# Kernel optimization log

Hardware: AMD Instinct MI355X
Metric: run time of the kernel (lower is better)

## Reference

```python
import jax, jax.numpy as jnp
import numpy as np
import math

IN_DIM = 256
OUT_DIM = 256
H = 4
DK = OUT_DIM // H  # 64
N = 40000
E = 300000
T = 2  # node types
R = 3  # relations: 0:(A->B), 1:(B->A), 2:(A->B)


def setup_inputs() -> dict:
    key = jax.random.key(0)
    ks = jax.random.split(key, 24)
    def xavier(k, shape):
        fan_in, fan_out = shape[-2], shape[-1]
        lim = math.sqrt(6.0 / (fan_in + fan_out))
        return jax.random.uniform(k, shape, jnp.float32, -lim, lim)
    inp = {
        "hA": jax.random.normal(ks[0], (N, IN_DIM), jnp.float32),
        "hB": jax.random.normal(ks[1], (N, IN_DIM), jnp.float32),
        "src0": jax.random.randint(ks[2], (E,), 0, N, jnp.int32),
        "dst0": jax.random.randint(ks[3], (E,), 0, N, jnp.int32),
        "src1": jax.random.randint(ks[4], (E,), 0, N, jnp.int32),
        "dst1": jax.random.randint(ks[5], (E,), 0, N, jnp.int32),
        "src2": jax.random.randint(ks[6], (E,), 0, N, jnp.int32),
        "dst2": jax.random.randint(ks[7], (E,), 0, N, jnp.int32),
        # per-node-type linear weights, stacked [T, in, out]
        "Wk": xavier(ks[8], (T, IN_DIM, OUT_DIM)),
        "bk": jnp.zeros((T, OUT_DIM), jnp.float32),
        "Wq": xavier(ks[9], (T, IN_DIM, OUT_DIM)),
        "bq": jnp.zeros((T, OUT_DIM), jnp.float32),
        "Wv": xavier(ks[10], (T, IN_DIM, OUT_DIM)),
        "bv": jnp.zeros((T, OUT_DIM), jnp.float32),
        "Wa": xavier(ks[11], (T, OUT_DIM, OUT_DIM)),
        "ba": jnp.zeros((T, OUT_DIM), jnp.float32),
        "rel_att": xavier(ks[12], (R, H, DK, DK)),
        "rel_msg": xavier(ks[13], (R, H, DK, DK)),
        "rel_pri": jnp.ones((R, H), jnp.float32),
        "skip": jnp.ones((T,), jnp.float32),
    }
    return inp


def _hgt_forward(hA, hB, Wk, bk, Wq, bq, Wv, bv, Wa, ba,
                 rel_att, rel_msg, rel_pri, skip, edges):
    h = [hA, hB]
    sqrt_dk = math.sqrt(DK)

    def proj(W, b, x, t):
        return (x @ W[t] + b[t]).reshape(-1, H, DK)

    def rel_agg(r, s, d, src, dst):
        # relation-specific transforms
        k = jnp.einsum('nhi,hij->nhj', proj(Wk, bk, h[s], s), rel_att[r])
        v = jnp.einsum('nhi,hij->nhj', proj(Wv, bv, h[s], s), rel_msg[r])
        q = proj(Wq, bq, h[d], d)
        nd = h[d].shape[0]
        # per-edge dot-product attention score [E, H]
        score = jnp.einsum('ehd,ehd->eh', q[dst], k[src]) * rel_pri[r] / sqrt_dk
        # edge softmax normalized by destination node
        m = jax.ops.segment_max(score, dst, num_segments=nd)
        e = jnp.exp(score - m[dst])
        denom = jax.ops.segment_sum(e, dst, num_segments=nd)
        attn = e / denom[dst]
        # weighted scatter-sum aggregation -> [nd, H, DK]
        return jax.ops.segment_sum(v[src] * attn[:, :, None], dst, num_segments=nd)

    (src0, dst0), (src1, dst1), (src2, dst2) = edges
    agg0 = rel_agg(0, 0, 1, src0, dst0)  # A -> B
    agg1 = rel_agg(1, 1, 0, src1, dst1)  # B -> A
    agg2 = rel_agg(2, 0, 1, src2, dst2)  # A -> B

    # cross_reducer='mean' over etypes per destination type
    t_A = agg1.reshape(-1, OUT_DIM)
    t_B = ((agg0 + agg2) * 0.5).reshape(-1, OUT_DIM)

    def ts_aggr(t, n_id, h_dst):
        alpha = jax.nn.sigmoid(skip[n_id])
        trans = t @ Wa[n_id] + ba[n_id]  # dropout p=0.0 -> identity
        return trans * alpha + h_dst * (1.0 - alpha)

    out_A = ts_aggr(t_A, 0, hA)
    out_B = ts_aggr(t_B, 1, hB)
    return jnp.stack([out_A, out_B])  # [2, N, OUT_DIM]


def reference(hA, hB, src0, dst0, src1, dst1, src2, dst2,
              Wk, bk, Wq, bq, Wv, bv, Wa, ba,
              rel_att, rel_msg, rel_pri, skip):
    edges = ((src0, dst0), (src1, dst1), (src2, dst2))
    return _hgt_forward(hA, hB, Wk, bk, Wq, bq, Wv, bv, Wa, ba,
                        rel_att, rel_msg, rel_pri, skip, edges)
```

## Files before the change

kernel.cpp:

```cpp
#include <hip/hip_runtime.h>

#define NN 40000
#define EE 300000
#define DIM 256
#define NHD 4
#define CAP 64

typedef __attribute__((ext_vector_type(8))) short bfrag;
typedef __attribute__((ext_vector_type(4))) float fx4;

static __device__ __forceinline__ float bf2f(unsigned short u) {
  union { unsigned int i; float f; } v; v.i = ((unsigned int)u) << 16; return v.f;
}
static __device__ __forceinline__ unsigned short f2bf(float f) {
  union { float f; unsigned int i; } v; v.f = f;
  unsigned int x = v.i;
  return (unsigned short)((x + 0x7fffu + ((x >> 16) & 1u)) >> 16);
}
static __device__ __forceinline__ void unpack4(uint2 u, float f[4]) {
  f[0] = bf2f((unsigned short)(u.x & 0xffffu));
  f[1] = bf2f((unsigned short)(u.x >> 16));
  f[2] = bf2f((unsigned short)(u.y & 0xffffu));
  f[3] = bf2f((unsigned short)(u.y >> 16));
}
static __device__ __forceinline__ void unpackKV(uint4 u, float k[4], float v[4]) {
  k[0] = bf2f((unsigned short)(u.x & 0xffffu)); k[1] = bf2f((unsigned short)(u.x >> 16));
  k[2] = bf2f((unsigned short)(u.y & 0xffffu)); k[3] = bf2f((unsigned short)(u.y >> 16));
  v[0] = bf2f((unsigned short)(u.z & 0xffffu)); v[1] = bf2f((unsigned short)(u.z >> 16));
  v[2] = bf2f((unsigned short)(u.w & 0xffffu)); v[3] = bf2f((unsigned short)(u.w >> 16));
}
static __device__ __forceinline__ void gload_lds16(const unsigned short* g, unsigned short* l) {
  __builtin_amdgcn_global_load_lds((const __attribute__((address_space(1))) void*)g,
                                   (__attribute__((address_space(3))) void*)l, 16, 0, 0);
}

#define LDSBUF 16384
static __device__ __forceinline__ void gemm_core(const unsigned short* __restrict__ X,
                                                 const unsigned short* __restrict__ WT,
                                                 int R0, int C0, int rowMax,
                                                 fx4 acc[4][4],
                                                 unsigned short* lds) {
  const int tid = threadIdx.x;
  const int wave = tid >> 6, lane = tid & 63;
  const int li = lane & 15, lk = lane >> 4;
  const int wr = wave >> 1, wc = wave & 1;
  const int lr = lane >> 3;
  const int swz = ((lane & 7) ^ lr) * 8;

#define STAGE(KT, BUF)                                                          \
  {                                                                             \
    unsigned short* lA = lds + (BUF) * LDSBUF;                                  \
    unsigned short* lB = lA + 8192;                                             \
    const int k0 = (KT) * 64;                                                   \
    _Pragma("unroll")                                                           \
    for (int i = 0; i < 4; ++i) {                                               \
      int g = wave * 4 + i;                                                     \
      int ra = min(R0 + g * 8 + lr, rowMax);                                    \
      gload_lds16(X + (size_t)ra * DIM + k0 + swz, lA + g * 512);               \
      int cb = C0 + g * 8 + lr;                                                 \
      gload_lds16(WT + (size_t)cb * DIM + k0 + swz, lB + g * 512);              \
    }                                                                           \
  }

  STAGE(0, 0);
#pragma unroll
  for (int kt = 0; kt < 4; ++kt) {
    __syncthreads();
    if (kt < 3) STAGE(kt + 1, (kt + 1) & 1);
    unsigned short* lA = lds + (kt & 1) * LDSBUF;
    unsigned short* lB = lA + 8192;
#pragma unroll
    for (int ks = 0; ks < 2; ++ks) {
      bfrag a[4], b[4];
      const int chb = (lk + ks * 4) ^ (li & 7);
#pragma unroll
      for (int mt = 0; mt < 4; ++mt)
        a[mt] = *(const bfrag*)(lA + (wr * 64 + mt * 16 + li) * 64 + chb * 8);
#pragma unroll
      for (int nt = 0; nt < 4; ++nt)
        b[nt] = *(const bfrag*)(lB + (wc * 64 + nt * 16 + li) * 64 + chb * 8);
#pragma unroll
      for (int mt = 0; mt < 4; ++mt)
#pragma unroll
        for (int nt = 0; nt < 4; ++nt)
          acc[mt][nt] = __builtin_amdgcn_mfma_f32_16x16x32_bf16(a[mt], b[nt], acc[mt][nt], 0, 0, 0);
    }
  }
#undef STAGE
}

__global__ __launch_bounds__(256) void cvt_kernel(const float* __restrict__ hA,
                                                  const float* __restrict__ hB,
                                                  unsigned short* __restrict__ XA,
                                                  unsigned short* __restrict__ XB) {
  long id = (long)blockIdx.x * 256 + threadIdx.x;
  const long half = (long)NN * DIM / 8;
  const float4* src; unsigned short* dst; long o;
  if (id < half) { src = (const float4*)hA; dst = XA; o = id; }
  else           { src = (const float4*)hB; dst = XB; o = id - half; }
  float4 a = src[o * 2], b = src[o * 2 + 1];
  uint4 pk;
  pk.x = (unsigned)f2bf(a.x) | ((unsigned)f2bf(a.y) << 16);
  pk.y = (unsigned)f2bf(a.z) | ((unsigned)f2bf(a.w) << 16);
  pk.z = (unsigned)f2bf(b.x) | ((unsigned)f2bf(b.y) << 16);
  pk.w = (unsigned)f2bf(b.z) | ((unsigned)f2bf(b.w) << 16);
  ((uint4*)dst)[o] = pk;
}

__global__ __launch_bounds__(256) void prep_weights(
    const float* __restrict__ Wk, const float* __restrict__ bk,
    const float* __restrict__ Wq, const float* __restrict__ bq,
    const float* __restrict__ Wv, const float* __restrict__ bv,
    const float* __restrict__ Wa,
    const float* __restrict__ rel_att, const float* __restrict__ rel_msg,
    const float* __restrict__ rel_pri,
    unsigned short* __restrict__ WT_A, unsigned short* __restrict__ WT_B,
    unsigned short* __restrict__ WaT, float* __restrict__ biasA, float* __restrict__ biasB) {
  int id = blockIdx.x * 256 + threadIdx.x;
  if (id < 262144) {
    int c = id >> 8, i = id & 255;
    int br = c >> 9, w = c & 511, h = w >> 7, ww = w & 127;
    int iskv = (ww >> 2) & 1;
    int j = (ww >> 3) * 4 + (ww & 3);
    int r = br ? 2 : 0;
    const float* W  = iskv ? Wv : Wk;
    const float* RM = iskv ? rel_msg : rel_att;
    const float* wrow = W + i * 256 + h * 64;
    const float* rm = RM + (size_t)((r * NHD + h) * 64) * 64 + j;
    float s = 0.f;
#pragma unroll 8
    for (int l = 0; l < 64; l++) s += wrow[l] * rm[l * 64];
    if (!iskv) s *= rel_pri[r * NHD + h] * 0.125f;
    WT_A[c * 256 + i] = f2bf(s);
    return;
  }
  id -= 262144;
  if (id < 65536) {
    int c = id >> 8, i = id & 255;
    WT_A[(1024 + c) * 256 + i] = f2bf(Wq[i * 256 + c]);
    return;
  }
  id -= 65536;
  if (id < 131072) {
    int c = id >> 8, i = id & 255;
    int h = c >> 7, ww = c & 127;
    int iskv = (ww >> 2) & 1;
    int j = (ww >> 3) * 4 + (ww & 3);
    const float* W  = iskv ? Wv : Wk;
    const float* RM = iskv ? rel_msg : rel_att;
    const float* wrow = W + 65536 + i * 256 + h * 64;
    const float* rm = RM + (size_t)((1 * NHD + h) * 64) * 64 + j;
    float s = 0.f;
#pragma unroll 8
    for (int l = 0; l < 64; l++) s += wrow[l] * rm[l * 64];
    if (!iskv) s *= rel_pri[1 * NHD + h] * 0.125f;
    WT_B[c * 256 + i] = f2bf(s);
    return;
  }
  id -= 131072;
  if (id < 65536) {
    int c = id >> 8, i = id & 255;
    WT_B[(512 + c) * 256 + i] = f2bf(Wq[65536 + i * 256 + c]);
    return;
  }
  id -= 65536;
  if (id < 131072) {
    int t = id >> 16, rem = id & 65535, c = rem >> 8, i = rem & 255;
    WaT[t * 65536 + c * 256 + i] = f2bf(Wa[t * 65536 + i * 256 + c]);
    return;
  }
  id -= 131072;
  if (id < 2048) {
    if (id < 1280) {
      int c = id; float s;
      if (c < 1024) {
        int br = c >> 9, w = c & 511, h = w >> 7, ww = w & 127;
        int iskv = (ww >> 2) & 1;
        int j = (ww >> 3) * 4 + (ww & 3);
        int r = br ? 2 : 0;
        const float* B  = iskv ? bv : bk;
        const float* RM = iskv ? rel_msg : rel_att;
        s = 0.f;
        for (int l = 0; l < 64; l++)
          s += B[h * 64 + l] * RM[(size_t)((r * NHD + h) * 64 + l) * 64 + j];
        if (!iskv) s *= rel_pri[r * NHD + h] * 0.125f;
      } else s = bq[c - 1024];
      biasA[c] = s;
    } else {
      int c = id - 1280; float s;
      if (c < 512) {
        int h = c >> 7, ww = c & 127;
        int iskv = (ww >> 2) & 1;
        int j = (ww >> 3) * 4 + (ww & 3);
        const float* B  = iskv ? bv : bk;
        const float* RM = iskv ? rel_msg : rel_att;
        s = 0.f;
        for (int l = 0; l < 64; l++)
          s += B[256 + h * 64 + l] * RM[(size_t)((1 * NHD + h) * 64 + l) * 64 + j];
        if (!iskv) s *= rel_pri[1 * NHD + h] * 0.125f;
      } else s = bq[256 + (c - 512)];
      biasB[c] = s;
    }
  }
}

__global__ __launch_bounds__(256) void bucket_build(const int* __restrict__ src0, const int* __restrict__ dst0,
                                                    const int* __restrict__ src1, const int* __restrict__ dst1,
                                                    const int* __restrict__ src2, const int* __restrict__ dst2,
                                                    int* __restrict__ cnt, int* __restrict__ bkt) {
  int e = blockIdx.x * 256 + threadIdx.x;
  if (e >= EE) return;
  int r = blockIdx.y;
  const int* src = r == 0 ? src0 : (r == 1 ? src1 : src2);
  const int* dst = r == 0 ? dst0 : (r == 1 ? dst1 : dst2);
  int d = dst[e];
  int pos = atomicAdd(&cnt[r * NN + d], 1);
  if (pos < CAP) bkt[(size_t)r * NN * CAP + d * CAP + pos] = src[e];
}

__global__ __launch_bounds__(256) void gemm_kvq(const unsigned short* __restrict__ X,
                                                const unsigned short* __restrict__ WT,
                                                const float* __restrict__ bias,
                                                unsigned short* __restrict__ Out, int ldOut) {
  __shared__ unsigned short lds[2 * LDSBUF];
  fx4 acc[4][4] = {};
  const int R0 = blockIdx.x * 128, C0 = blockIdx.y * 128;
  gemm_core(X, WT, R0, C0, NN - 1, acc, lds);
  const int wave = threadIdx.x >> 6, lane = threadIdx.x & 63;
  const int li = lane & 15, lk = lane >> 4;
  const int wr = wave >> 1, wc = wave & 1;
#pragma unroll
  for (int mt = 0; mt < 4; mt++)
#pragma unroll
    for (int nt = 0; nt < 4; nt++) {
      int col = C0 + wc * 64 + nt * 16 + li;
      float bcol = bias[col];
      int rbase = R0 + wr * 64 + mt * 16 + lk * 4;
#pragma unroll
      for (int i = 0; i < 4; i++) {
        int row = rbase + i;
        if (row < NN) Out[(long)row * ldOut + col] = f2bf(acc[mt][nt][i] + bcol);
      }
    }
}

__global__ __launch_bounds__(256) void agg_all(const unsigned short* __restrict__ OutA,
                                               const unsigned short* __restrict__ OutB,
                                               const int* __restrict__ cnt,
                                               const int* __restrict__ bkt,
                                               unsigned short* __restrict__ tA,
                                               unsigned short* __restrict__ tB) {
  int wid = (blockIdx.x * 256 + threadIdx.x) >> 6;
  int lane = threadIdx.x & 63;
  int h = lane >> 4, li = lane & 15;
  int qoff = h * 64 + li * 4;
  int kvoff = h * 128 + li * 8;
  if (wid < NN) {
    int n = wid;
    float q[4]; unpack4(*(const uint2*)(OutB + (size_t)n * 768 + 512 + qoff), q);
    int c0 = min(cnt[n], CAP);
    int c2 = min(cnt[2 * NN + n], CAP);
    int s0 = (lane < c0) ? bkt[(size_t)0 * NN * CAP + n * CAP + lane] : 0;
    int s2 = (lane < c2) ? bkt[(size_t)2 * NN * CAP + n * CAP + lane] : 0;
    float l0 = 0.f, l2 = 0.f;
    float b00 = 0.f, b01 = 0.f, b02 = 0.f, b03 = 0.f;
    float b20 = 0.f, b21 = 0.f, b22 = 0.f, b23 = 0.f;
    int cm = max(c0, c2);
    for (int e = 0; e < cm; ++e) {
      if (e < c0) {
        int src = __builtin_amdgcn_readlane(s0, e);
        uint4 u = *(const uint4*)(OutA + (size_t)src * 1280 + kvoff);
        float kk[4], vv[4]; unpackKV(u, kk, vv);
        float pp = q[0] * kk[0] + q[1] * kk[1] + q[2] * kk[2] + q[3] * kk[3];
        pp += __shfl_xor(pp, 1); pp += __shfl_xor(pp, 2);
        pp += __shfl_xor(pp, 4); pp += __shfl_xor(pp, 8);
        float p = __expf(pp);
        l0 += p; b00 += p * vv[0]; b01 += p * vv[1]; b02 += p * vv[2]; b03 += p * vv[3];
      }
      if (e < c2) {
        int src = __builtin_amdgcn_readlane(s2, e);
        uint4 u = *(const uint4*)(OutA + (size_t)src * 1280 + 512 + kvoff);
        float kk[4], vv[4]; unpackKV(u, kk, vv);
        float pp = q[0] * kk[0] + q[1] * kk[1] + q[2] * kk[2] + q[3] * kk[3];
        pp += __shfl_xor(pp, 1); pp += __shfl_xor(pp, 2);
        pp += __shfl_xor(pp, 4); pp += __shfl_xor(pp, 8);
        float p = __expf(pp);
        l2 += p; b20 += p * vv[0]; b21 += p * vv[1]; b22 += p * vv[2]; b23 += p * vv[3];
      }
    }
    float i0 = (l0 > 0.f) ? 0.5f / l0 : 0.f;
    float i2 = (l2 > 0.f) ? 0.5f / l2 : 0.f;
    float r0 = b00 * i0 + b20 * i2, r1 = b01 * i0 + b21 * i2;
    float r2 = b02 * i0 + b22 * i2, r3 = b03 * i0 + b23 * i2;
    uint2 pk;
    pk.x = (unsigned)f2bf(r0) | ((unsigned)f2bf(r1) << 16);
    pk.y = (unsigned)f2bf(r2) | ((unsigned)f2bf(r3) << 16);
    *(uint2*)(tB + (size_t)n * DIM + qoff) = pk;
  } else if (wid < 2 * NN) {
    int n = wid - NN;
    float q[4]; unpack4(*(const uint2*)(OutA + (size_t)n * 1280 + 1024 + qoff), q);
    int c = min(cnt[NN + n], CAP);
    int s1 = (lane < c) ? bkt[(size_t)1 * NN * CAP + n * CAP + lane] : 0;
    float l = 0.f, a0 = 0.f, a1 = 0.f, a2 = 0.f, a3 = 0.f;
    int e = 0;
    for (; e + 1 < c; e += 2) {
      int sa = __builtin_amdgcn_readlane(s1, e);
      int sb = __builtin_amdgcn_readlane(s1, e + 1);
      uint4 ua = *(const uint4*)(OutB + (size_t)sa * 768 + kvoff);
      uint4 ub = *(const uint4*)(OutB + (size_t)sb * 768 + kvoff);
      float ka[4], va[4], kb[4], vb[4];
      unpackKV(ua, ka, va); unpackKV(ub, kb, vb);
      float pa = q[0] * ka[0] + q[1] * ka[1] + q[2] * ka[2] + q[3] * ka[3];
      float pb = q[0] * kb[0] + q[1] * kb[1] + q[2] * kb[2] + q[3] * kb[3];
      pa += __shfl_xor(pa, 1); pa += __shfl_xor(pa, 2);
      pa += __shfl_xor(pa, 4); pa += __shfl_xor(pa, 8);
      pb += __shfl_xor(pb, 1); pb += __shfl_xor(pb, 2);
      pb += __shfl_xor(pb, 4); pb += __shfl_xor(pb, 8);
      pa = __expf(pa); pb = __expf(pb);
      l += pa; l += pb;
      a0 += pa * va[0]; a1 += pa * va[1]; a2 += pa * va[2]; a3 += pa * va[3];
      a0 += pb * vb[0]; a1 += pb * vb[1]; a2 += pb * vb[2]; a3 += pb * vb[3];
    }
    if (e < c) {
      int sa = __builtin_amdgcn_readlane(s1, e);
      uint4 ua = *(const uint4*)(OutB + (size_t)sa * 768 + kvoff);
      float ka[4], va[4]; unpackKV(ua, ka, va);
      float pa = q[0] * ka[0] + q[1] * ka[1] + q[2] * ka[2] + q[3] * ka[3];
      pa += __shfl_xor(pa, 1); pa += __shfl_xor(pa, 2);
      pa += __shfl_xor(pa, 4); pa += __shfl_xor(pa, 8);
      pa = __expf(pa);
      l += pa;
      a0 += pa * va[0]; a1 += pa * va[1]; a2 += pa * va[2]; a3 += pa * va[3];
    }
    float inv = (l > 0.f) ? 1.f / l : 0.f;
    uint2 pk;
    pk.x = (unsigned)f2bf(a0 * inv) | ((unsigned)f2bf(a1 * inv) << 16);
    pk.y = (unsigned)f2bf(a2 * inv) | ((unsigned)f2bf(a3 * inv) << 16);
    *(uint2*)(tA + (size_t)n * DIM + qoff) = pk;
  }
}

__global__ __launch_bounds__(256) void gemm_final2(const unsigned short* __restrict__ tA,
                                                   const unsigned short* __restrict__ tB,
                                                   const unsigned short* __restrict__ XA,
                                                   const unsigned short* __restrict__ XB,
                                                   const unsigned short* __restrict__ WaT,
                                                   const float* __restrict__ ba,
                                                   const float* __restrict__ skip,
                                                   float* __restrict__ outp) {
  __shared__ unsigned short lds[2 * LDSBUF];
  const int t = blockIdx.z;
  const unsigned short* Tt = t ? tB : tA;
  const unsigned short* hin = t ? XB : XA;
  float* op = outp + (size_t)t * NN * DIM;
  fx4 acc[4][4] = {};
  const int R0 = blockIdx.x * 128, C0 = blockIdx.y * 128;
  gemm_core(Tt, WaT + t * 65536, R0, C0, NN - 1, acc, lds);
  const int wave = threadIdx.x >> 6, lane = threadIdx.x & 63;
  const int li = lane & 15, lk = lane >> 4;
  const int wr = wave >> 1, wc = wave & 1;
  float alpha = 1.f / (1.f + __expf(-skip[t]));
  float beta = 1.f - alpha;
#pragma unroll
  for (int mt = 0; mt < 4; mt++)
#pragma unroll
    for (int nt = 0; nt < 4; nt++) {
      int col = C0 + wc * 64 + nt * 16 + li;
      float bcol = ba[t * 256 + col];
      int rbase = R0 + wr * 64 + mt * 16 + lk * 4;
#pragma unroll
      for (int i = 0; i < 4; i++) {
        int row = rbase + i;
        if (row < NN) {
          float hv = bf2f(hin[(size_t)row * DIM + col]);
          op[(long)row * DIM + col] = (acc[mt][nt][i] + bcol) * alpha + hv * beta;
        }
      }
    }
}

extern "C" void kernel_launch(void* const* d_in, const int* in_sizes, int n_in,
                              void* d_out, int out_size, void* d_ws, size_t ws_size,
                              hipStream_t stream) {
  const float* hA = (const float*)d_in[0];
  const float* hB = (const float*)d_in[1];
  const int* src0 = (const int*)d_in[2];
  const int* dst0 = (const int*)d_in[3];
  const int* src1 = (const int*)d_in[4];
  const int* dst1 = (const int*)d_in[5];
  const int* src2 = (const int*)d_in[6];
  const int* dst2 = (const int*)d_in[7];
  const float* Wk = (const float*)d_in[8];
  const float* bk = (const float*)d_in[9];
  const float* Wq = (const float*)d_in[10];
  const float* bq = (const float*)d_in[11];
  const float* Wv = (const float*)d_in[12];
  const float* bv = (const float*)d_in[13];
  const float* Wa = (const float*)d_in[14];
  const float* ba = (const float*)d_in[15];
  const float* rel_att = (const float*)d_in[16];
  const float* rel_msg = (const float*)d_in[17];
  const float* rel_pri = (const float*)d_in[18];
  const float* skip = (const float*)d_in[19];

  char* w = (char*)d_ws;
  unsigned short* XA   = (unsigned short*)(w);
  unsigned short* XB   = (unsigned short*)(w + 20480000);
  unsigned short* OutA = (unsigned short*)(w + 40960000);
  unsigned short* OutB = (unsigned short*)(w + 143360000);
  unsigned short* WT_A = (unsigned short*)(w + 204800000);
  unsigned short* WT_B = (unsigned short*)(w + 205455360);
  unsigned short* WaT  = (unsigned short*)(w + 205848576);
  float* biasA = (float*)(w + 206110720);
  float* biasB = (float*)(w + 206115840);
  int* cnt  = (int*)(w + 206118912);
  int* bkt  = (int*)(w + 206598912);
  unsigned short* tA = (unsigned short*)(w + 237318912);
  unsigned short* tB = (unsigned short*)(w + 257798912);

  hipMemsetAsync(cnt, 0, 3 * NN * sizeof(int), stream);
  cvt_kernel<<<10000, 256, 0, stream>>>(hA, hB, XA, XB);
  prep_weights<<<2568, 256, 0, stream>>>(Wk, bk, Wq, bq, Wv, bv, Wa,
                                         rel_att, rel_msg, rel_pri,
                                         WT_A, WT_B, WaT, biasA, biasB);
  bucket_build<<<dim3((EE + 255) / 256, 3), 256, 0, stream>>>(src0, dst0, src1, dst1, src2, dst2, cnt, bkt);
  gemm_kvq<<<dim3(313, 10), 256, 0, stream>>>(XA, WT_A, biasA, OutA, 1280);
  gemm_kvq<<<dim3(313, 6), 256, 0, stream>>>(XB, WT_B, biasB, OutB, 768);
  agg_all<<<20000, 256, 0, stream>>>(OutA, OutB, cnt, bkt, tA, tB);
  gemm_final2<<<dim3(313, 2, 2), 256, 0, stream>>>(tA, tB, XA, XB, WaT, ba, skip, (float*)d_out);
}
```

Measured before the change: 441.2 us.

## Shrink GEMM row tiles to 64 and software-pipeline gathers in aggregation

The GEMM kernels now use 64-row tiles with a single LDS buffer and no double-buffered prefetch. Because 40000 divides evenly by 64, the row bounds checks are dropped, and the grid doubles to fill more CUs with lower LDS use per block. The aggregation kernel now issues K/V gathers for the next edges before processing the current ones, two or four deep, to hide gather latency. The trade-off is losing the overlap of global-to-LDS loads with MFMA inside each GEMM block.

```diff
diff --git a/kernel.cpp b/kernel.cpp
--- a/kernel.cpp
+++ b/kernel.cpp
@@ -34,59 +34,46 @@
                                    (__attribute__((address_space(3))) void*)l, 16, 0, 0);
 }
 
-#define LDSBUF 16384
-static __device__ __forceinline__ void gemm_core(const unsigned short* __restrict__ X,
-                                                 const unsigned short* __restrict__ WT,
-                                                 int R0, int C0, int rowMax,
-                                                 fx4 acc[4][4],
-                                                 unsigned short* lds) {
+static __device__ __forceinline__ void gemm_core64(const unsigned short* __restrict__ X,
+                                                   const unsigned short* __restrict__ WT,
+                                                   int R0, int C0,
+                                                   fx4 acc[2][4],
+                                                   unsigned short* ldsA,
+                                                   unsigned short* ldsB) {
   const int tid = threadIdx.x;
   const int wave = tid >> 6, lane = tid & 63;
   const int li = lane & 15, lk = lane >> 4;
   const int wr = wave >> 1, wc = wave & 1;
   const int lr = lane >> 3;
   const int swz = ((lane & 7) ^ lr) * 8;
-
-#define STAGE(KT, BUF)                                                          \
-  {                                                                             \
-    unsigned short* lA = lds + (BUF) * LDSBUF;                                  \
-    unsigned short* lB = lA + 8192;                                             \
-    const int k0 = (KT) * 64;                                                   \
-    _Pragma("unroll")                                                           \
-    for (int i = 0; i < 4; ++i) {                                               \
-      int g = wave * 4 + i;                                                     \
-      int ra = min(R0 + g * 8 + lr, rowMax);                                    \
-      gload_lds16(X + (size_t)ra * DIM + k0 + swz, lA + g * 512);               \
-      int cb = C0 + g * 8 + lr;                                                 \
-      gload_lds16(WT + (size_t)cb * DIM + k0 + swz, lB + g * 512);              \
-    }                                                                           \
-  }
-
-  STAGE(0, 0);
 #pragma unroll
   for (int kt = 0; kt < 4; ++kt) {
+    const int k0 = kt * 64;
+    if (kt) __syncthreads();
+#pragma unroll
+    for (int i = 0; i < 6; ++i) {
+      int g = wave * 6 + i;
+      if (g < 8) gload_lds16(X + (size_t)(R0 + g * 8 + lr) * DIM + k0 + swz, ldsA + g * 512);
+      else       gload_lds16(WT + (size_t)(C0 + (g - 8) * 8 + lr) * DIM + k0 + swz, ldsB + (g - 8) * 512);
+    }
     __syncthreads();
-    if (kt < 3) STAGE(kt + 1, (kt + 1) & 1);
-    unsigned short* lA = lds + (kt & 1) * LDSBUF;
-    unsigned short* lB = lA + 8192;
 #pragma unroll
     for (int ks = 0; ks < 2; ++ks) {
-      bfrag a[4], b[4];
+      bfrag a[2], b[4];
       const int chb = (lk + ks * 4) ^ (li & 7);
 #pragma unroll
-      for (int mt = 0; mt < 4; ++mt)
-        a[mt] = *(const bfrag*)(lA + (wr * 64 + mt * 16 + li) * 64 + chb * 8);
+      for (int mt = 0; mt < 2; ++mt)
+        a[mt] = *(const bfrag*)(ldsA + (wr * 32 + mt * 16 + li) * 64 + chb * 8);
 #pragma unroll
       for (int nt = 0; nt < 4; ++nt)
-        b[nt] = *(const bfrag*)(lB + (wc * 64 + nt * 16 + li) * 64 + chb * 8);
-#pragma unroll
-      for (int mt = 0; mt < 4; ++mt)
+        b[nt] = *(const bfrag*)(ldsB + (wc * 64 + nt * 16 + li) * 64 + chb * 8);
+#pragma unroll
+      for (int mt = 0; mt < 2; ++mt)
 #pragma unroll
         for (int nt = 0; nt < 4; ++nt)
           acc[mt][nt] = __builtin_amdgcn_mfma_f32_16x16x32_bf16(a[mt], b[nt], acc[mt][nt], 0, 0, 0);
     }
   }
-#undef STAGE
 }
 
 __global__ __launch_bounds__(256) void cvt_kernel(const float* __restrict__ hA,
@@ -222,27 +209,33 @@
                                                 const unsigned short* __restrict__ WT,
                                                 const float* __restrict__ bias,
                                                 unsigned short* __restrict__ Out, int ldOut) {
-  __shared__ unsigned short lds[2 * LDSBUF];
-  fx4 acc[4][4] = {};
-  const int R0 = blockIdx.x * 128, C0 = blockIdx.y * 128;
-  gemm_core(X, WT, R0, C0, NN - 1, acc, lds);
+  __shared__ unsigned short ldsA[4096], ldsB[8192];
+  fx4 acc[2][4] = {};
+  const int R0 = blockIdx.x * 64, C0 = blockIdx.y * 128;
+  gemm_core64(X, WT, R0, C0, acc, ldsA, ldsB);
   const int wave = threadIdx.x >> 6, lane = threadIdx.x & 63;
   const int li = lane & 15, lk = lane >> 4;
   const int wr = wave >> 1, wc = wave & 1;
 #pragma unroll
-  for (int mt = 0; mt < 4; mt++)
+  for (int mt = 0; mt < 2; mt++)
 #pragma unroll
     for (int nt = 0; nt < 4; nt++) {
       int col = C0 + wc * 64 + nt * 16 + li;
       float bcol = bias[col];
-      int rbase = R0 + wr * 64 + mt * 16 + lk * 4;
-#pragma unroll
-      for (int i = 0; i < 4; i++) {
-        int row = rbase + i;
-        if (row < NN) Out[(long)row * ldOut + col] = f2bf(acc[mt][nt][i] + bcol);
-      }
-    }
-}
+      int rbase = R0 + wr * 32 + mt * 16 + lk * 4;
+#pragma unroll
+      for (int i = 0; i < 4; i++)
+        Out[(long)(rbase + i) * ldOut + col] = f2bf(acc[mt][nt][i] + bcol);
+    }
+}
+
+#define PROC(U, L, BX, BY, BZ, BW)                                              \
+  { float kk[4], vv[4]; unpackKV(U, kk, vv);                                    \
+    float pp = q[0]*kk[0] + q[1]*kk[1] + q[2]*kk[2] + q[3]*kk[3];               \
+    pp += __shfl_xor(pp, 1); pp += __shfl_xor(pp, 2);                           \
+    pp += __shfl_xor(pp, 4); pp += __shfl_xor(pp, 8);                           \
+    float p = __expf(pp);                                                       \
+    L += p; BX += p*vv[0]; BY += p*vv[1]; BZ += p*vv[2]; BW += p*vv[3]; }
 
 __global__ __launch_bounds__(256) void agg_all(const unsigned short* __restrict__ OutA,
                                                const unsigned short* __restrict__ OutB,
@@ -255,87 +248,75 @@
   int h = lane >> 4, li = lane & 15;
   int qoff = h * 64 + li * 4;
   int kvoff = h * 128 + li * 8;
+  const uint4 Z = {0u, 0u, 0u, 0u};
   if (wid < NN) {
     int n = wid;
     float q[4]; unpack4(*(const uint2*)(OutB + (size_t)n * 768 + 512 + qoff), q);
     int c0 = min(cnt[n], CAP);
     int c2 = min(cnt[2 * NN + n], CAP);
-    int s0 = (lane < c0) ? bkt[(size_t)0 * NN * CAP + n * CAP + lane] : 0;
+    int s0 = (lane < c0) ? bkt[(size_t)n * CAP + lane] : 0;
     int s2 = (lane < c2) ? bkt[(size_t)2 * NN * CAP + n * CAP + lane] : 0;
-    float l0 = 0.f, l2 = 0.f;
-    float b00 = 0.f, b01 = 0.f, b02 = 0.f, b03 = 0.f;
-    float b20 = 0.f, b21 = 0.f, b22 = 0.f, b23 = 0.f;
+#define LDK0(E) (*(const uint4*)(OutA + (size_t)__builtin_amdgcn_readlane(s0, (E) & 63) * 1280 + kvoff))
+#define LDK2(E) (*(const uint4*)(OutA + (size_t)__builtin_amdgcn_readlane(s2, (E) & 63) * 1280 + 512 + kvoff))
+    float l0 = 0.f, b00 = 0.f, b01 = 0.f, b02 = 0.f, b03 = 0.f;
+    float l2 = 0.f, b20 = 0.f, b21 = 0.f, b22 = 0.f, b23 = 0.f;
     int cm = max(c0, c2);
-    for (int e = 0; e < cm; ++e) {
-      if (e < c0) {
-        int src = __builtin_amdgcn_readlane(s0, e);
-        uint4 u = *(const uint4*)(OutA + (size_t)src * 1280 + kvoff);
-        float kk[4], vv[4]; unpackKV(u, kk, vv);
-        float pp = q[0] * kk[0] + q[1] * kk[1] + q[2] * kk[2] + q[3] * kk[3];
-        pp += __shfl_xor(pp, 1); pp += __shfl_xor(pp, 2);
-        pp += __shfl_xor(pp, 4); pp += __shfl_xor(pp, 8);
-        float p = __expf(pp);
-        l0 += p; b00 += p * vv[0]; b01 += p * vv[1]; b02 += p * vv[2]; b03 += p * vv[3];
-      }
-      if (e < c2) {
-        int src = __builtin_amdgcn_readlane(s2, e);
-        uint4 u = *(const uint4*)(OutA + (size_t)src * 1280 + 512 + kvoff);
-        float kk[4], vv[4]; unpackKV(u, kk, vv);
-        float pp = q[0] * kk[0] + q[1] * kk[1] + q[2] * kk[2] + q[3] * kk[3];
-        pp += __shfl_xor(pp, 1); pp += __shfl_xor(pp, 2);
-        pp += __shfl_xor(pp, 4); pp += __shfl_xor(pp, 8);
-        float p = __expf(pp);
-        l2 += p; b20 += p * vv[0]; b21 += p * vv[1]; b22 += p * vv[2]; b23 += p * vv[3];
-      }
+    uint4 a0 = Z, a2 = Z, d0 = Z, d2 = Z;
+    if (0 < c0) a0 = LDK0(0);
+    if (0 < c2) a2 = LDK2(0);
+    if (1 < c0) d0 = LDK0(1);
+    if (1 < c2) d2 = LDK2(1);
+    for (int e = 0; e < cm; e += 2) {
+      uint4 p0 = Z, p2 = Z, r0 = Z, r2 = Z;
+      if (e + 2 < c0) p0 = LDK0(e + 2);
+      if (e + 2 < c2) p2 = LDK2(e + 2);
+      if (e + 3 < c0) r0 = LDK0(e + 3);
+      if (e + 3 < c2) r2 = LDK2(e + 3);
+      if (e < c0) PROC(a0, l0, b00, b01, b02, b03);
+      if (e < c2) PROC(a2, l2, b20, b21, b22, b23);
+      if (e + 1 < c0) PROC(d0, l0, b00, b01, b02, b03);
+      if (e + 1 < c2) PROC(d2, l2, b20, b21, b22, b23);
+      a0 = p0; a2 = p2; d0 = r0; d2 = r2;
     }
     float i0 = (l0 > 0.f) ? 0.5f / l0 : 0.f;
     float i2 = (l2 > 0.f) ? 0.5f / l2 : 0.f;
-    float r0 = b00 * i0 + b20 * i2, r1 = b01 * i0 + b21 * i2;
-    float r2 = b02 * i0 + b22 * i2, r3 = b03 * i0 + b23 * i2;
+    float r0f = b00 * i0 + b20 * i2, r1f = b01 * i0 + b21 * i2;
+    float r2f = b02 * i0 + b22 * i2, r3f = b03 * i0 + b23 * i2;
     uint2 pk;
-    pk.x = (unsigned)f2bf(r0) | ((unsigned)f2bf(r1) << 16);
-    pk.y = (unsigned)f2bf(r2) | ((unsigned)f2bf(r3) << 16);
+    pk.x = (unsigned)f2bf(r0f) | ((unsigned)f2bf(r1f) << 16);
+    pk.y = (unsigned)f2bf(r2f) | ((unsigned)f2bf(r3f) << 16);
     *(uint2*)(tB + (size_t)n * DIM + qoff) = pk;
+#undef LDK0
+#undef LDK2
   } else if (wid < 2 * NN) {
     int n = wid - NN;
     float q[4]; unpack4(*(const uint2*)(OutA + (size_t)n * 1280 + 1024 + qoff), q);
     int c = min(cnt[NN + n], CAP);
-    int s1 = (lane < c) ? bkt[(size_t)1 * NN * CAP + n * CAP + lane] : 0;
-    float l = 0.f, a0 = 0.f, a1 = 0.f, a2 = 0.f, a3 = 0.f;
-    int e = 0;
-    for (; e + 1 < c; e += 2) {
-      int sa = __builtin_amdgcn_readlane(s1, e);
-      int sb = __builtin_amdgcn_readlane(s1, e + 1);
-      uint4 ua = *(const uint4*)(OutB + (size_t)sa * 768 + kvoff);
-      uint4 ub = *(const uint4*)(OutB + (size_t)sb * 768 + kvoff);
-      float ka[4], va[4], kb[4], vb[4];
-      unpackKV(ua, ka, va); unpackKV(ub, kb, vb);
-      float pa = q[0] * ka[0] + q[1] * ka[1] + q[2] * ka[2] + q[3] * ka[3];
-      float pb = q[0] * kb[0] + q[1] * kb[1] + q[2] * kb[2] + q[3] * kb[3];
-      pa += __shfl_xor(pa, 1); pa += __shfl_xor(pa, 2);
-      pa += __shfl_xor(pa, 4); pa += __shfl_xor(pa, 8);
-      pb += __shfl_xor(pb, 1); pb += __shfl_xor(pb, 2);
-      pb += __shfl_xor(pb, 4); pb += __shfl_xor(pb, 8);
-      pa = __expf(pa); pb = __expf(pb);
-      l += pa; l += pb;
-      a0 += pa * va[0]; a1 += pa * va[1]; a2 += pa * va[2]; a3 += pa * va[3];
-      a0 += pb * vb[0]; a1 += pb * vb[1]; a2 += pb * vb[2]; a3 += pb * vb[3];
-    }
-    if (e < c) {
-      int sa = __builtin_amdgcn_readlane(s1, e);
-      uint4 ua = *(const uint4*)(OutB + (size_t)sa * 768 + kvoff);
-      float ka[4], va[4]; unpackKV(ua, ka, va);
-      float pa = q[0] * ka[0] + q[1] * ka[1] + q[2] * ka[2] + q[3] * ka[3];
-      pa += __shfl_xor(pa, 1); pa += __shfl_xor(pa, 2);
-      pa += __shfl_xor(pa, 4); pa += __shfl_xor(pa, 8);
-      pa = __expf(pa);
-      l += pa;
-      a0 += pa * va[0]; a1 += pa * va[1]; a2 += pa * va[2]; a3 += pa * va[3];
-    }
+    int s1 = (lane < c) ? bkt[(size_t)NN * CAP + n * CAP + lane] : 0;
+#define LDK1(E) (*(const uint4*)(OutB + (size_t)__builtin_amdgcn_readlane(s1, (E) & 63) * 768 + kvoff))
+    float l = 0.f, a0f = 0.f, a1f = 0.f, a2f = 0.f, a3f = 0.f;
+    uint4 e0 = Z, e1 = Z, e2 = Z, e3 = Z;
+    if (0 < c) e0 = LDK1(0);
+    if (1 < c) e1 = LDK1(1);
+    if (2 < c) e2 = LDK1(2);
+    if (3 < c) e3 = LDK1(3);
+    for (int e = 0; e < c; e += 4) {
+      uint4 f0 = Z, f1 = Z, f2 = Z, f3 = Z;
+      if (e + 4 < c) f0 = LDK1(e + 4);
+      if (e + 5 < c) f1 = LDK1(e + 5);
+      if (e + 6 < c) f2 = LDK1(e + 6);
+      if (e + 7 < c) f3 = LDK1(e + 7);
+      PROC(e0, l, a0f, a1f, a2f, a3f);
+      if (e + 1 < c) PROC(e1, l, a0f, a1f, a2f, a3f);
+      if (e + 2 < c) PROC(e2, l, a0f, a1f, a2f, a3f);
+      if (e + 3 < c) PROC(e3, l, a0f, a1f, a2f, a3f);
+      e0 = f0; e1 = f1; e2 = f2; e3 = f3;
+    }
+#undef LDK1
     float inv = (l > 0.f) ? 1.f / l : 0.f;
     uint2 pk;
-    pk.x = (unsigned)f2bf(a0 * inv) | ((unsigned)f2bf(a1 * inv) << 16);
-    pk.y = (unsigned)f2bf(a2 * inv) | ((unsigned)f2bf(a3 * inv) << 16);
+    pk.x = (unsigned)f2bf(a0f * inv) | ((unsigned)f2bf(a1f * inv) << 16);
+    pk.y = (unsigned)f2bf(a2f * inv) | ((unsigned)f2bf(a3f * inv) << 16);
     *(uint2*)(tA + (size_t)n * DIM + qoff) = pk;
   }
 }
@@ -348,33 +329,31 @@
                                                    const float* __restrict__ ba,
                                                    const float* __restrict__ skip,
                                                    float* __restrict__ outp) {
-  __shared__ unsigned short lds[2 * LDSBUF];
+  __shared__ unsigned short ldsA[4096], ldsB[8192];
   const int t = blockIdx.z;
   const unsigned short* Tt = t ? tB : tA;
   const unsigned short* hin = t ? XB : XA;
   float* op = outp + (size_t)t * NN * DIM;
-  fx4 acc[4][4] = {};
-  const int R0 = blockIdx.x * 128, C0 = blockIdx.y * 128;
-  gemm_core(Tt, WaT + t * 65536, R0, C0, NN - 1, acc, lds);
+  fx4 acc[2][4] = {};
+  const int R0 = blockIdx.x * 64, C0 = blockIdx.y * 128;
+  gemm_core64(Tt, WaT + t * 65536, R0, C0, acc, ldsA, ldsB);
   const int wave = threadIdx.x >> 6, lane = threadIdx.x & 63;
   const int li = lane & 15, lk = lane >> 4;
   const int wr = wave >> 1, wc = wave & 1;
   float alpha = 1.f / (1.f + __expf(-skip[t]));
   float beta = 1.f - alpha;
 #pragma unroll
-  for (int mt = 0; mt < 4; mt++)
+  for (int mt = 0; mt < 2; mt++)
 #pragma unroll
     for (int nt = 0; nt < 4; nt++) {
       int col = C0 + wc * 64 + nt * 16 + li;
       float bcol = ba[t * 256 + col];
-      int rbase = R0 + wr * 64 + mt * 16 + lk * 4;
+      int rbase = R0 + wr * 32 + mt * 16 + lk * 4;
 #pragma unroll
       for (int i = 0; i < 4; i++) {
         int row = rbase + i;
-        if (row < NN) {
-          float hv = bf2f(hin[(size_t)row * DIM + col]);
-          op[(long)row * DIM + col] = (acc[mt][nt][i] + bcol) * alpha + hv * beta;
-        }
+        float hv = bf2f(hin[(size_t)row * DIM + col]);
+        op[(long)row * DIM + col] = (acc[mt][nt][i] + bcol) * alpha + hv * beta;
       }
     }
 }
@@ -424,8 +403,8 @@
                                          rel_att, rel_msg, rel_pri,
                                          WT_A, WT_B, WaT, biasA, biasB);
   bucket_build<<<dim3((EE + 255) / 256, 3), 256, 0, stream>>>(src0, dst0, src1, dst1, src2, dst2, cnt, bkt);
-  gemm_kvq<<<dim3(313, 10), 256, 0, stream>>>(XA, WT_A, biasA, OutA, 1280);
-  gemm_kvq<<<dim3(313, 6), 256, 0, stream>>>(XB, WT_B, biasB, OutB, 768);
+  gemm_kvq<<<dim3(625, 10), 256, 0, stream>>>(XA, WT_A, biasA, OutA, 1280);
+  gemm_kvq<<<dim3(625, 6), 256, 0, stream>>>(XB, WT_B, biasB, OutB, 768);
   agg_all<<<20000, 256, 0, stream>>>(OutA, OutB, cnt, bkt, tA, tB);
-  gemm_final2<<<dim3(313, 2, 2), 256, 0, stream>>>(tA, tB, XA, XB, WaT, ba, skip, (float*)d_out);
-}
+  gemm_final2<<<dim3(625, 2, 2), 256, 0, stream>>>(tA, tB, XA, XB, WaT, ba, skip, (float*)d_out);
+}
```

Result: faster. 371.9 us (-15.7%).
